# Kernel tuning notes

Hardware: AMD Instinct MI355X
Metric: run time of the kernel (lower is better)

The kernel has to match this reference:

```python
import jax, jax.numpy as jnp
import numpy as np

N = 100000      # nodes
E = 1600000     # edges (before self-loops)
IN_DIM = 128
HEADS = 4
C = 32          # hid_dim // heads = 128 // 4
SLOPE = 0.2     # PyG GATConv default negative_slope


def setup_inputs() -> dict:
    key = jax.random.key(0)
    k1, k2, k3, k4, k5 = jax.random.split(key, 5)
    x = jax.random.normal(k1, (N, IN_DIM), dtype=jnp.float32)
    edge_index = jax.random.randint(k2, (2, E), 0, N, dtype=jnp.int32)
    # learned parameters of GATConv
    W = jax.random.normal(k3, (IN_DIM, HEADS * C), dtype=jnp.float32) / np.sqrt(IN_DIM)
    att_src = jax.random.normal(k4, (HEADS, C), dtype=jnp.float32) * 0.1
    att_dst = jax.random.normal(k5, (HEADS, C), dtype=jnp.float32) * 0.1
    bias = jnp.zeros((HEADS * C,), dtype=jnp.float32)
    return {"x": x, "edge_index": edge_index, "W": W,
            "att_src": att_src, "att_dst": att_dst, "bias": bias}


def reference(x, edge_index, W, att_src, att_dst, bias):
    # PyG GATConv default add_self_loops=True
    loops = jnp.arange(N, dtype=edge_index.dtype)
    ei = jnp.concatenate([edge_index, jnp.stack([loops, loops])], axis=1)
    src, dst = ei[0], ei[1]                       # messages flow src -> dst

    h = (x @ W).reshape(N, HEADS, C)              # [N,H,C]
    a_src = jnp.einsum('nhc,hc->nh', h, att_src)  # [N,H]
    a_dst = jnp.einsum('nhc,hc->nh', h, att_dst)  # [N,H]

    e = a_src[src] + a_dst[dst]                   # [E+N,H] per-edge logits
    e = jax.nn.leaky_relu(e, SLOPE)

    # segment softmax over edges sharing a destination node
    m = jax.ops.segment_max(e, dst, num_segments=N)        # [N,H]
    e = jnp.exp(e - m[dst])
    s = jax.ops.segment_sum(e, dst, num_segments=N)        # [N,H]
    alpha = e / (s[dst] + 1e-16)                            # [E+N,H]

    msg = h[src] * alpha[:, :, None]                        # [E+N,H,C]
    out = jax.ops.segment_sum(msg, dst, num_segments=N)     # [N,H,C]
    return out.reshape(N, HEADS * C) + bias                 # concat heads + bias
```

## Files before the change

kernel.cpp:

```cpp
#include <hip/hip_runtime.h>
#include <cstddef>

#define HEADS 4
#define HC 128
#define SLOPE 0.2f
#define NPBUCK 256
#define NSBMAX 512
#define SBCAP 5120
#define CHUNK 4096

using half8 = __attribute__((ext_vector_type(8))) _Float16;
using f32x4 = __attribute__((ext_vector_type(4))) float;

__device__ __forceinline__ float edge_w(float v) {
    v = v > 0.f ? v : SLOPE * v;
    return __expf(v);
}

__global__ void wt_kernel(const float* __restrict__ W, _Float16* __restrict__ WTh) {
    int k = threadIdx.x;
    int nn = blockIdx.x;
    WTh[nn * HC + k] = (_Float16)W[k * HC + nn];
}

__global__ __launch_bounds__(256)
void gemm_att_count_kernel(const float* __restrict__ x, const _Float16* __restrict__ WTh,
                           const float* __restrict__ att_src, const float* __restrict__ att_dst,
                           _Float16* __restrict__ h2,
                           float* __restrict__ a_s, float* __restrict__ a_d,
                           const int* __restrict__ ei, int* __restrict__ cnt2d,
                           int gb, int E, int n) {
    __shared__ int cnt[NSBMAX];
    int tid = threadIdx.x;

    if (blockIdx.x >= gb) {
        int cb = blockIdx.x - gb;
        for (int i = tid; i < NSBMAX; i += 256) cnt[i] = 0;
        __syncthreads();
        int Etot = E + n;
        int e0 = cb * CHUNK;
        int eend = e0 + CHUNK; if (eend > Etot) eend = Etot;
        for (int e = e0 + tid; e < eend; e += 256) {
            int dst = (e < E) ? ei[E + e] : (e - E);
            atomicAdd(&cnt[dst >> 8], 1);
        }
        __syncthreads();
        int* row = cnt2d + (size_t)cb * NSBMAX;
        for (int i = tid; i < NSBMAX; i += 256) row[i] = cnt[i];
        return;
    }

    int wv   = tid >> 6;
    int lane = tid & 63;
    int t    = lane & 15;
    int q    = lane >> 4;
    int r0   = blockIdx.x * 64 + wv * 16;

    f32x4 acc[8];
#pragma unroll
    for (int ct = 0; ct < 8; ++ct) acc[ct] = (f32x4){0.f, 0.f, 0.f, 0.f};

    int  arow = r0 + t;
    bool aval = arow < n;
    const float* xp = x + (size_t)(aval ? arow : 0) * HC;

    for (int kc = 0; kc < 4; ++kc) {
        int k0 = kc * 32 + q * 8;
        half8 a;
        float4 fa = *(const float4*)(xp + k0);
        float4 fb = *(const float4*)(xp + k0 + 4);
        if (!aval) { fa = make_float4(0.f,0.f,0.f,0.f); fb = fa; }
        a[0] = (_Float16)fa.x; a[1] = (_Float16)fa.y;
        a[2] = (_Float16)fa.z; a[3] = (_Float16)fa.w;
        a[4] = (_Float16)fb.x; a[5] = (_Float16)fb.y;
        a[6] = (_Float16)fb.z; a[7] = (_Float16)fb.w;
#pragma unroll
        for (int ct = 0; ct < 8; ++ct) {
            half8 b = *(const half8*)(WTh + (size_t)(ct * 16 + t) * HC + k0);
            acc[ct] = __builtin_amdgcn_mfma_f32_16x16x32_f16(a, b, acc[ct], 0, 0, 0);
        }
    }

#pragma unroll
    for (int reg = 0; reg < 4; ++reg) {
        int row = r0 + q * 4 + reg;
        if (row < n) {
#pragma unroll
            for (int ct = 0; ct < 8; ++ct)
                h2[(size_t)row * HC + ct * 16 + t] = (_Float16)acc[ct][reg];
        }
    }

    float asv[8], adv[8];
#pragma unroll
    for (int ct = 0; ct < 8; ++ct) {
        asv[ct] = att_src[ct * 16 + t];
        adv[ct] = att_dst[ct * 16 + t];
    }
#pragma unroll
    for (int reg = 0; reg < 4; ++reg) {
        int row = r0 + q * 4 + reg;
        float4 ps, pd;
        ps.x = acc[0][reg]*asv[0] + acc[1][reg]*asv[1];
        ps.y = acc[2][reg]*asv[2] + acc[3][reg]*asv[3];
        ps.z = acc[4][reg]*asv[4] + acc[5][reg]*asv[5];
        ps.w = acc[6][reg]*asv[6] + acc[7][reg]*asv[7];
        pd.x = acc[0][reg]*adv[0] + acc[1][reg]*adv[1];
        pd.y = acc[2][reg]*adv[2] + acc[3][reg]*adv[3];
        pd.z = acc[4][reg]*adv[4] + acc[5][reg]*adv[5];
        pd.w = acc[6][reg]*adv[6] + acc[7][reg]*adv[7];
#pragma unroll
        for (int m = 1; m < 16; m <<= 1) {
            ps.x += __shfl_xor(ps.x, m); ps.y += __shfl_xor(ps.y, m);
            ps.z += __shfl_xor(ps.z, m); ps.w += __shfl_xor(ps.w, m);
            pd.x += __shfl_xor(pd.x, m); pd.y += __shfl_xor(pd.y, m);
            pd.z += __shfl_xor(pd.z, m); pd.w += __shfl_xor(pd.w, m);
        }
        if (t == 0 && row < n) {
            ((float4*)a_s)[row] = ps;
            ((float4*)a_d)[row] = pd;
        }
    }
}

__global__ __launch_bounds__(512)
void colscan_kernel(const int* __restrict__ cnt2d, int* __restrict__ base2d,
                    int* __restrict__ bucketend, int nchunks) {
    __shared__ int tmp[512];
    int b = blockIdx.x;
    int t = threadIdx.x;
    int v = (t < nchunks) ? cnt2d[(size_t)t * NSBMAX + b] : 0;
    tmp[t] = v;
    __syncthreads();
#pragma unroll
    for (int off = 1; off < 512; off <<= 1) {
        int u = (t >= off) ? tmp[t - off] : 0;
        __syncthreads();
        tmp[t] += u;
        __syncthreads();
    }
    if (t < nchunks) base2d[(size_t)t * NSBMAX + b] = b * SBCAP + tmp[t] - v;
    if (t == 511) bucketend[b] = b * SBCAP + tmp[511];
}

__global__ __launch_bounds__(256)
void scatter_kernel(const int* __restrict__ ei, int E, int n,
                    const int* __restrict__ base2d, int2* __restrict__ binned) {
    __shared__ int cur[NSBMAX];
    int tid = threadIdx.x;
    const int* row = base2d + (size_t)blockIdx.x * NSBMAX;
    for (int i = tid; i < NSBMAX; i += 256) cur[i] = row[i];
    __syncthreads();
    int Etot = E + n;
    int e0 = blockIdx.x * CHUNK;
    int eend = e0 + CHUNK; if (eend > Etot) eend = Etot;
    for (int e = e0 + tid; e < eend; e += 256) {
        int src, dst;
        if (e < E) { src = ei[e]; dst = ei[E + e]; }
        else       { src = e - E; dst = src; }
        int p = atomicAdd(&cur[dst >> 8], 1);
        binned[p] = make_int2(src, dst);
    }
}

__global__ __launch_bounds__(256)
void place_kernel(const int* __restrict__ bucketend, const int2* __restrict__ binned,
                  int* __restrict__ sorted, int* __restrict__ rowstart,
                  int* __restrict__ deg, int n) {
    __shared__ int cnt[256];
    __shared__ int pos[256];
    int b = blockIdx.x;
    int dst0 = b << 8;
    int rows = n - dst0; if (rows > 256) rows = 256;
    int tid = threadIdx.x;

    cnt[tid] = 0;
    __syncthreads();
    int wstart = b * SBCAP;
    int wend   = bucketend[b];
    for (int e = wstart + tid; e < wend; e += 256)
        atomicAdd(&cnt[binned[e].y - dst0], 1);
    __syncthreads();

    int d = cnt[tid];
    pos[tid] = d;
    __syncthreads();
#pragma unroll
    for (int off = 1; off < 256; off <<= 1) {
        int v = (tid >= off) ? pos[tid - off] : 0;
        __syncthreads();
        pos[tid] += v;
        __syncthreads();
    }
    int excl = pos[tid] - d;
    if (tid < rows) {
        rowstart[dst0 + tid] = wstart + excl;
        deg[dst0 + tid] = d;
    }
    cnt[tid] = excl;
    __syncthreads();
    for (int e = wstart + tid; e < wend; e += 256) {
        int2 ed = binned[e];
        int p = atomicAdd(&cnt[ed.y - dst0], 1);
        sorted[wstart + p] = ed.x;
    }
}

__global__ __launch_bounds__(256)
void agg_kernel(const int* __restrict__ rowstart, const int* __restrict__ deg,
                const int* __restrict__ sorted,
                const float* __restrict__ a_s, const float* __restrict__ a_d,
                const _Float16* __restrict__ h2, const float* __restrict__ bias,
                float* __restrict__ out, int n) {
    int dst = blockIdx.x * 16 + (threadIdx.x >> 4);
    if (dst >= n) return;
    int li   = threadIdx.x & 15;
    int head = li >> 2;
    int start = rowstart[dst];
    int cntv  = deg[dst];

    float ad = a_d[(size_t)dst * 4 + head];
    const uint4* h4 = (const uint4*)h2;
    float acc[8] = {0.f,0.f,0.f,0.f,0.f,0.f,0.f,0.f};
    float wsum = 0.f;

    for (int j = 0; j < cntv; j += 4) {
        int sv[4]; float wv[4];
#pragma unroll
        for (int k = 0; k < 4; ++k) {
            int idx = j + k;
            bool valid = idx < cntv;
            sv[k] = sorted[start + (valid ? idx : 0)];
            wv[k] = valid ? 1.f : 0.f;
        }
        uint4 hv[4];
#pragma unroll
        for (int k = 0; k < 4; ++k)
            hv[k] = h4[(size_t)sv[k] * 16 + li];
        float as[4];
#pragma unroll
        for (int k = 0; k < 4; ++k)
            as[k] = a_s[(size_t)sv[k] * 4 + head];
#pragma unroll
        for (int k = 0; k < 4; ++k) {
            float w = wv[k] * edge_w(as[k] + ad);
            union { uint4 u; _Float16 f[8]; } hc; hc.u = hv[k];
#pragma unroll
            for (int c = 0; c < 8; ++c)
                acc[c] = fmaf((float)hc.f[c], w, acc[c]);
            wsum += w;
        }
    }

    float inv = 1.f / wsum;
    float4 b0 = ((const float4*)bias)[li * 2];
    float4 b1 = ((const float4*)bias)[li * 2 + 1];
    float4 o0 = make_float4(acc[0]*inv + b0.x, acc[1]*inv + b0.y,
                            acc[2]*inv + b0.z, acc[3]*inv + b0.w);
    float4 o1 = make_float4(acc[4]*inv + b1.x, acc[5]*inv + b1.y,
                            acc[6]*inv + b1.z, acc[7]*inv + b1.w);
    float4* op = (float4*)(out + (size_t)dst * HC);
    op[li * 2]     = o0;
    op[li * 2 + 1] = o1;
}

extern "C" void kernel_launch(void* const* d_in, const int* in_sizes, int n_in,
                              void* d_out, int out_size, void* d_ws, size_t ws_size,
                              hipStream_t stream) {
    const float* x       = (const float*)d_in[0];
    const int*   ei      = (const int*)d_in[1];
    const float* W       = (const float*)d_in[2];
    const float* att_src = (const float*)d_in[3];
    const float* att_dst = (const float*)d_in[4];
    const float* bias    = (const float*)d_in[5];

    int n = in_sizes[0] / HC;
    int E = in_sizes[1] / 2;
    int Etot = E + n;
    int nbuck   = (n + NPBUCK - 1) / NPBUCK;
    int nchunks = (Etot + CHUNK - 1) / CHUNK;
    int gb      = (n + 63) / 64;

    _Float16* h2     = (_Float16*)d_ws;
    _Float16* WTh    = h2 + (size_t)n * HC;
    float* a_s       = (float*)(WTh + HC * HC);
    float* a_d       = a_s + (size_t)n * HEADS;
    int*   cnt2d     = (int*)(a_d + (size_t)n * HEADS);
    int*   base2d    = cnt2d + (size_t)nchunks * NSBMAX;
    int*   bucketend = base2d + (size_t)nchunks * NSBMAX;
    int*   rowstart  = bucketend + NSBMAX;
    int*   deg       = rowstart + n;
    int2*  binned    = (int2*)(deg + n);
    int*   sorted    = (int*)(binned + (size_t)nbuck * SBCAP);
    float* out       = (float*)d_out;

    wt_kernel<<<HC, HC, 0, stream>>>(W, WTh);
    gemm_att_count_kernel<<<gb + nchunks, 256, 0, stream>>>(
        x, WTh, att_src, att_dst, h2, a_s, a_d, ei, cnt2d, gb, E, n);
    colscan_kernel<<<nbuck, 512, 0, stream>>>(cnt2d, base2d, bucketend, nchunks);
    scatter_kernel<<<nchunks, 256, 0, stream>>>(ei, E, n, base2d, binned);
    place_kernel<<<nbuck, 256, 0, stream>>>(bucketend, binned, sorted,
                                            rowstart, deg, n);
    agg_kernel<<<(n + 15) / 16, 256, 0, stream>>>(rowstart, deg, sorted,
                                                  a_s, a_d, h2, bias, out, n);
}
```

Before: 266.7 us.

## Pack binned edges into one int and pad CSR rows for vector index loads

Binned edges are now stored as a single packed int, with src in the low 17 bits and the local dst offset in the high bits, instead of an int2. This halves the traffic of the scatter and place passes. Place zero-fills each bucket and pads every row's start to a multiple of 4. That lets the aggregation kernel load neighbor indices with int4 vector loads and process 8 edges per iteration, masking the extras by weight. The risks are that the packing assumes fewer than 2^17 nodes and the larger SBCAP must absorb the padding. The 8-wide reads can also run past the end of a row, and for the last bucket past the end of the sorted array.

New measurement: 270.4 us. About the same (+1.4%).

```diff
diff --git a/kernel.cpp b/kernel.cpp
--- a/kernel.cpp
+++ b/kernel.cpp
@@ -6,7 +6,7 @@
 #define SLOPE 0.2f
 #define NPBUCK 256
 #define NSBMAX 512
-#define SBCAP 5120
+#define SBCAP 5376
 #define CHUNK 4096
 
 using half8 = __attribute__((ext_vector_type(8))) _Float16;
@@ -145,7 +145,7 @@
 
 __global__ __launch_bounds__(256)
 void scatter_kernel(const int* __restrict__ ei, int E, int n,
-                    const int* __restrict__ base2d, int2* __restrict__ binned) {
+                    const int* __restrict__ base2d, int* __restrict__ binned) {
     __shared__ int cur[NSBMAX];
     int tid = threadIdx.x;
     const int* row = base2d + (size_t)blockIdx.x * NSBMAX;
@@ -159,12 +159,12 @@
         if (e < E) { src = ei[e]; dst = ei[E + e]; }
         else       { src = e - E; dst = src; }
         int p = atomicAdd(&cur[dst >> 8], 1);
-        binned[p] = make_int2(src, dst);
+        binned[p] = src | ((dst & 255) << 17);
     }
 }
 
 __global__ __launch_bounds__(256)
-void place_kernel(const int* __restrict__ bucketend, const int2* __restrict__ binned,
+void place_kernel(const int* __restrict__ bucketend, const int* __restrict__ binned,
                   int* __restrict__ sorted, int* __restrict__ rowstart,
                   int* __restrict__ deg, int n) {
     __shared__ int cnt[256];
@@ -173,17 +173,20 @@
     int dst0 = b << 8;
     int rows = n - dst0; if (rows > 256) rows = 256;
     int tid = threadIdx.x;
-
-    cnt[tid] = 0;
-    __syncthreads();
     int wstart = b * SBCAP;
     int wend   = bucketend[b];
+
+    for (int e = wstart + tid; e < wstart + SBCAP; e += 256) sorted[e] = 0;
+
+    cnt[tid] = 0;
+    __syncthreads();
     for (int e = wstart + tid; e < wend; e += 256)
-        atomicAdd(&cnt[binned[e].y - dst0], 1);
-    __syncthreads();
-
-    int d = cnt[tid];
-    pos[tid] = d;
+        atomicAdd(&cnt[binned[e] >> 17], 1);
+    __syncthreads();
+
+    int d   = cnt[tid];
+    int dAl = (d + 3) & ~3;
+    pos[tid] = dAl;
     __syncthreads();
 #pragma unroll
     for (int off = 1; off < 256; off <<= 1) {
@@ -192,17 +195,17 @@
         pos[tid] += v;
         __syncthreads();
     }
-    int excl = pos[tid] - d;
+    int exclAl = pos[tid] - dAl;
     if (tid < rows) {
-        rowstart[dst0 + tid] = wstart + excl;
+        rowstart[dst0 + tid] = wstart + exclAl;
         deg[dst0 + tid] = d;
     }
-    cnt[tid] = excl;
+    cnt[tid] = exclAl;
     __syncthreads();
     for (int e = wstart + tid; e < wend; e += 256) {
-        int2 ed = binned[e];
-        int p = atomicAdd(&cnt[ed.y - dst0], 1);
-        sorted[wstart + p] = ed.x;
+        int v = binned[e];
+        int p = atomicAdd(&cnt[v >> 17], 1);
+        sorted[wstart + p] = v & 0x1FFFF;
     }
 }
 
@@ -224,26 +227,22 @@
     float acc[8] = {0.f,0.f,0.f,0.f,0.f,0.f,0.f,0.f};
     float wsum = 0.f;
 
-    for (int j = 0; j < cntv; j += 4) {
-        int sv[4]; float wv[4];
-#pragma unroll
-        for (int k = 0; k < 4; ++k) {
-            int idx = j + k;
-            bool valid = idx < cntv;
-            sv[k] = sorted[start + (valid ? idx : 0)];
-            wv[k] = valid ? 1.f : 0.f;
-        }
-        uint4 hv[4];
-#pragma unroll
-        for (int k = 0; k < 4; ++k)
+    for (int j = 0; j < cntv; j += 8) {
+        const int* sp = sorted + start + j;
+        int4 sa = *(const int4*)sp;
+        int4 sb = *(const int4*)(sp + 4);
+        int sv[8] = {sa.x, sa.y, sa.z, sa.w, sb.x, sb.y, sb.z, sb.w};
+        uint4 hv[8];
+#pragma unroll
+        for (int k = 0; k < 8; ++k)
             hv[k] = h4[(size_t)sv[k] * 16 + li];
-        float as[4];
-#pragma unroll
-        for (int k = 0; k < 4; ++k)
+        float as[8];
+#pragma unroll
+        for (int k = 0; k < 8; ++k)
             as[k] = a_s[(size_t)sv[k] * 4 + head];
 #pragma unroll
-        for (int k = 0; k < 4; ++k) {
-            float w = wv[k] * edge_w(as[k] + ad);
+        for (int k = 0; k < 8; ++k) {
+            float w = (j + k < cntv) ? edge_w(as[k] + ad) : 0.f;
             union { uint4 u; _Float16 f[8]; } hc; hc.u = hv[k];
 #pragma unroll
             for (int c = 0; c < 8; ++c)
@@ -290,8 +289,8 @@
     int*   bucketend = base2d + (size_t)nchunks * NSBMAX;
     int*   rowstart  = bucketend + NSBMAX;
     int*   deg       = rowstart + n;
-    int2*  binned    = (int2*)(deg + n);
-    int*   sorted    = (int*)(binned + (size_t)nbuck * SBCAP);
+    int*   binned    = deg + n;
+    int*   sorted    = binned + (size_t)nbuck * SBCAP;
     float* out       = (float*)d_out;
 
     wt_kernel<<<HC, HC, 0, stream>>>(W, WTh);
```
